# Kernel tuning notes

Measured on AMD Instinct MI355X. Metric: run time of the kernel, lower is better.

## Reference

```python
import jax, jax.numpy as jnp
import numpy as np

B, S, D, O = 1, 2048, 512, 512
H, QD, K, PK = 8, 256, 16, 256
N = PK * PK  # 65536 experts
HALF = QD // 2  # sub-query dim per product-key dimension


def _l2norm(x):
    # matches F.normalize(dim=-1): x / max(||x||, 1e-12)
    n = jnp.sqrt(jnp.sum(x * x, axis=-1, keepdims=True))
    return x / jnp.maximum(n, 1e-12)


def setup_inputs() -> dict:
    key = jax.random.key(0)
    ks = jax.random.split(key, 9)
    return {
        "hidden_states": jax.random.normal(ks[0], (B, S, D), jnp.float32),
        "Wq": jax.random.normal(ks[1], (H * QD, D), jnp.float32) * 0.02,
        "bq": jnp.zeros((H * QD,), jnp.float32),
        "ln_g": jnp.ones((QD,), jnp.float32),
        "ln_b": jnp.zeros((QD,), jnp.float32),
        "keys0": jax.random.normal(ks[2], (PK, HALF), jnp.float32) * 0.02,
        "keys1": jax.random.normal(ks[3], (PK, HALF), jnp.float32) * 0.02,
        "expert_down": jax.random.normal(ks[4], (N, D), jnp.float32) * 0.02,
        "expert_up": jax.random.normal(ks[5], (N, O), jnp.float32) * 0.02,
    }


def reference(hidden_states, Wq, bq, ln_g, ln_b, keys0, keys1, expert_down, expert_up):
    b, s, d = hidden_states.shape
    # query projection + layernorm over query_dim
    q = (hidden_states @ Wq.T + bq).reshape(b, s, H, QD)
    mu = jnp.mean(q, axis=-1, keepdims=True)
    var = jnp.mean((q - mu) ** 2, axis=-1, keepdims=True)
    q = (q - mu) / jnp.sqrt(var + 1e-5) * ln_g + ln_b
    # split into per-dimension sub-queries, normalize queries and keys
    q0, q1 = q[..., :HALF], q[..., HALF:]
    s0 = jnp.einsum('bshq,eq->bshe', _l2norm(q0), _l2norm(keys0))  # [b,s,H,PK]
    s1 = jnp.einsum('bshq,eq->bshe', _l2norm(q1), _l2norm(keys1))
    # per-dim top-k' (k' = K=16 here due to clamping logic in source)
    sc0, ix0 = jax.lax.top_k(s0, K)
    sc1, ix1 = jax.lax.top_k(s1, K)
    # combinatorial merge: scores add; NOTE source adds indices with multiplier 1
    # for the last dim and never scales the first-dim indices (faithful repro).
    cs = (sc0[..., :, None] + sc1[..., None, :]).reshape(b, s, H, K * K)
    ci = (ix0[..., :, None] + ix1[..., None, :]).reshape(b, s, H, K * K)
    fs, pos = jax.lax.top_k(cs, K)
    fi = jnp.take_along_axis(ci, pos, axis=-1)  # [b,s,H,K] expert ids
    w = jax.nn.softmax(fs, axis=-1)
    # gather rank-1 experts and apply: down-project, gelu, up-project, combine
    down = expert_down[fi]  # [b,s,H,K,D]
    up = expert_up[fi]      # [b,s,H,K,O]
    inner = jnp.einsum('bsd,bshkd->bshk', hidden_states, down)
    act = jax.nn.gelu(inner, approximate=False)
    out = jnp.einsum('bshk,bshko->bso', act * w, up)
    return out
```

## Files before the change

kernel.cpp:

```cpp
#include <hip/hip_runtime.h>
#include <math.h>

constexpr int Sx    = 2048;
constexpr int Dx    = 512;
constexpr int Hx    = 8;
constexpr int QDx   = 256;
constexpr int HALFx = 128;
constexpr int PKx   = 256;
constexpr int Kx    = 16;
constexpr int HQx   = Hx * QDx;
constexpr int Rx    = Sx * Hx;
constexpr int Ox    = 512;
constexpr int NEXP  = 511;

__device__ __forceinline__ unsigned short f2bf(float x) {
    unsigned u = __float_as_uint(x);
    unsigned r = (u + 0x7FFFu + ((u >> 16) & 1u)) >> 16;
    return (unsigned short)r;
}
__device__ __forceinline__ float bf2f(unsigned short h) {
    return __uint_as_float(((unsigned)h) << 16);
}

__global__ __launch_bounds__(64) void knorm_kernel(
    const float* __restrict__ k0, const float* __restrict__ k1,
    float* __restrict__ k0n, float* __restrict__ k1n)
{
    const int row = blockIdx.x;
    const float* src = (row < PKx) ? (k0 + (size_t)row * HALFx)
                                   : (k1 + (size_t)(row - PKx) * HALFx);
    float* dst = (row < PKx) ? (k0n + (size_t)row * HALFx)
                             : (k1n + (size_t)(row - PKx) * HALFx);
    const int t = threadIdx.x;
    float a = src[t];
    float b = src[t + 64];
    float ss = a * a + b * b;
#pragma unroll
    for (int off = 32; off; off >>= 1) ss += __shfl_xor(ss, off);
    float n = fmaxf(sqrtf(ss), 1e-12f);
    dst[t]      = a / n;
    dst[t + 64] = b / n;
}

__global__ __launch_bounds__(256) void conv_kernel(
    const float* __restrict__ src, unsigned short* __restrict__ dst, int n4)
{
    int i = blockIdx.x * 256 + threadIdx.x;
    if (i >= n4) return;
    float4 v = ((const float4*)src)[i];
    ((ushort4*)dst)[i] = make_ushort4(f2bf(v.x), f2bf(v.y), f2bf(v.z), f2bf(v.w));
}

__global__ __launch_bounds__(256) void gemm128_kernel(
    const float* __restrict__ A, int lda,
    const float* __restrict__ B, int ldb,
    const float* __restrict__ bias,
    float* __restrict__ C, int ldc, int K)
{
    constexpr int BM = 128, BN = 64, BK = 32;
    constexpr int ASTR = BM + 4;
    constexpr int BSTR = BN + 4;
    __shared__ __align__(16) float As[BK * ASTR];
    __shared__ __align__(16) float Bs[BK * BSTR];
    const int tid = threadIdx.x;
    const int bm = blockIdx.y * BM;
    const int bn = blockIdx.x * BN;

    const int sq = tid & 7;
    const int sr = tid >> 3;
    const int m0 = (tid >> 4) * 8;
    const int n0 = (tid & 15) * 4;

    float4 pa[4], pb[2];
#pragma unroll
    for (int i = 0; i < 4; ++i)
        pa[i] = *(const float4*)&A[(size_t)(bm + sr + i * 32) * lda + sq * 4];
#pragma unroll
    for (int i = 0; i < 2; ++i)
        pb[i] = *(const float4*)&B[(size_t)(bn + sr + i * 32) * ldb + sq * 4];

    float acc[8][4] = {{0.f}};
    const int niter = K / BK;
    for (int it = 0; it < niter; ++it) {
        __syncthreads();
#pragma unroll
        for (int i = 0; i < 4; ++i) {
            const float v[4] = {pa[i].x, pa[i].y, pa[i].z, pa[i].w};
#pragma unroll
            for (int j = 0; j < 4; ++j)
                As[(sq * 4 + j) * ASTR + sr + i * 32] = v[j];
        }
#pragma unroll
        for (int i = 0; i < 2; ++i) {
            const float v[4] = {pb[i].x, pb[i].y, pb[i].z, pb[i].w};
#pragma unroll
            for (int j = 0; j < 4; ++j)
                Bs[(sq * 4 + j) * BSTR + sr + i * 32] = v[j];
        }
        __syncthreads();
        if (it + 1 < niter) {
            const int ko = (it + 1) * BK;
#pragma unroll
            for (int i = 0; i < 4; ++i)
                pa[i] = *(const float4*)&A[(size_t)(bm + sr + i * 32) * lda + ko + sq * 4];
#pragma unroll
            for (int i = 0; i < 2; ++i)
                pb[i] = *(const float4*)&B[(size_t)(bn + sr + i * 32) * ldb + ko + sq * 4];
        }
#pragma unroll
        for (int k = 0; k < BK; ++k) {
            float af[8], bf[4];
            *(float4*)&af[0] = *(const float4*)&As[k * ASTR + m0];
            *(float4*)&af[4] = *(const float4*)&As[k * ASTR + m0 + 4];
            *(float4*)&bf[0] = *(const float4*)&Bs[k * BSTR + n0];
#pragma unroll
            for (int i = 0; i < 8; ++i)
#pragma unroll
                for (int j = 0; j < 4; ++j)
                    acc[i][j] = fmaf(af[i], bf[j], acc[i][j]);
        }
    }
    float4 bv = make_float4(0.f, 0.f, 0.f, 0.f);
    if (bias) bv = *(const float4*)&bias[bn + n0];
#pragma unroll
    for (int i = 0; i < 8; ++i) {
        float4 o;
        o.x = acc[i][0] + bv.x;
        o.y = acc[i][1] + bv.y;
        o.z = acc[i][2] + bv.z;
        o.w = acc[i][3] + bv.w;
        *(float4*)&C[(size_t)(bm + m0 + i) * ldc + bn + n0] = o;
    }
}

__global__ __launch_bounds__(256) void ln_kernel(
    float* __restrict__ q, const float* __restrict__ g,
    const float* __restrict__ b)
{
    const int r = blockIdx.x * 4 + (threadIdx.x >> 6);
    float* row = q + (size_t)r * QDx;
    const int t = threadIdx.x & 63;
    float v0 = row[t], v1 = row[t + 64], v2 = row[t + 128], v3 = row[t + 192];
    float sum = v0 + v1 + v2 + v3;
#pragma unroll
    for (int off = 32; off; off >>= 1) sum += __shfl_xor(sum, off);
    const float mu = sum * (1.f / 256.f);
    float d0 = v0 - mu, d1 = v1 - mu, d2 = v2 - mu, d3 = v3 - mu;
    float ss = d0 * d0 + d1 * d1 + d2 * d2 + d3 * d3;
#pragma unroll
    for (int off = 32; off; off >>= 1) ss += __shfl_xor(ss, off);
    const float var = ss * (1.f / 256.f);
    const float inv = 1.0f / sqrtf(var + 1e-5f);
    v0 = d0 * inv * g[t]       + b[t];
    v1 = d1 * inv * g[t + 64]  + b[t + 64];
    v2 = d2 * inv * g[t + 128] + b[t + 128];
    v3 = d3 * inv * g[t + 192] + b[t + 192];
    float s0 = v0 * v0 + v1 * v1;
#pragma unroll
    for (int off = 32; off; off >>= 1) s0 += __shfl_xor(s0, off);
    float n0 = fmaxf(sqrtf(s0), 1e-12f);
    float s1 = v2 * v2 + v3 * v3;
#pragma unroll
    for (int off = 32; off; off >>= 1) s1 += __shfl_xor(s1, off);
    float n1 = fmaxf(sqrtf(s1), 1e-12f);
    row[t]       = v0 / n0;
    row[t + 64]  = v1 / n0;
    row[t + 128] = v2 / n1;
    row[t + 192] = v3 / n1;
}

__device__ __forceinline__ unsigned fkey(float f) {
    unsigned u = __float_as_uint(f);
    return u ^ ((u & 0x80000000u) ? 0xFFFFFFFFu : 0x80000000u);
}

__device__ __forceinline__ void extract16(
    const float v[4], const unsigned u[4], unsigned T, int lane,
    unsigned long long lmask, float* outv, int* outi)
{
    unsigned long long mg[4];
    int gt_total = 0;
#pragma unroll
    for (int j = 0; j < 4; ++j) {
        mg[j] = __ballot(u[j] > T);
        gt_total += __popcll(mg[j]);
    }
    int bg = 0, be = gt_total;
#pragma unroll
    for (int j = 0; j < 4; ++j) {
        unsigned long long me = __ballot(u[j] == T);
        int idx = lane + 64 * j;
        if (u[j] > T) {
            int pg = bg + __popcll(mg[j] & lmask);
            outv[pg] = v[j]; outi[pg] = idx;
        } else if (u[j] == T) {
            int pe = be + __popcll(me & lmask);
            if (pe < 16) { outv[pe] = v[j]; outi[pe] = idx; }
        }
        bg += __popcll(mg[j]);
        be += __popcll(me);
    }
}

__global__ __launch_bounds__(256) void topk_kernel(
    const float* __restrict__ s0g, const float* __restrict__ s1g,
    int* __restrict__ fib, float* __restrict__ wb)
{
    __shared__ float sc0[4][Kx], sc1[4][Kx], fsv[4][Kx];
    __shared__ int ix0[4][Kx], ix1[4][Kx], fid[4][Kx];
    const int w = threadIdx.x >> 6;
    const int r = blockIdx.x * 4 + w;
    const int lane = threadIdx.x & 63;
    const unsigned long long lmask = (1ull << lane) - 1ull;

    float v0[4], v1[4];
    unsigned u0[4], u1[4];
#pragma unroll
    for (int j = 0; j < 4; ++j) {
        v0[j] = s0g[(size_t)r * PKx + lane + 64 * j];
        v1[j] = s1g[(size_t)r * PKx + lane + 64 * j];
        u0[j] = fkey(v0[j]);
        u1[j] = fkey(v1[j]);
    }

    unsigned T0 = 0, T1 = 0;
    for (int bit = 31; bit >= 0; --bit) {
        const unsigned c0 = T0 | (1u << bit);
        const unsigned c1 = T1 | (1u << bit);
        int n0 = 0, n1 = 0;
#pragma unroll
        for (int j = 0; j < 4; ++j) {
            n0 += __popcll(__ballot(u0[j] >= c0));
            n1 += __popcll(__ballot(u1[j] >= c1));
        }
        if (n0 >= Kx) T0 = c0;
        if (n1 >= Kx) T1 = c1;
    }
    extract16(v0, u0, T0, lane, lmask, &sc0[w][0], &ix0[w][0]);
    extract16(v1, u1, T1, lane, lmask, &sc1[w][0], &ix1[w][0]);
    __syncthreads();

    float cv[4];
    unsigned cu[4];
    int ci[4];
#pragma unroll
    for (int j = 0; j < 4; ++j) {
        int p = lane + 64 * j;
        cv[j] = sc0[w][p >> 4] + sc1[w][p & 15];
        cu[j] = fkey(cv[j]);
        ci[j] = ix0[w][p >> 4] + ix1[w][p & 15];
    }
    unsigned T2 = 0;
    for (int bit = 31; bit >= 0; --bit) {
        const unsigned c2 = T2 | (1u << bit);
        int n2 = 0;
#pragma unroll
        for (int j = 0; j < 4; ++j) n2 += __popcll(__ballot(cu[j] >= c2));
        if (n2 >= Kx) T2 = c2;
    }
    {
        unsigned long long mg[4];
        int gt_total = 0;
#pragma unroll
        for (int j = 0; j < 4; ++j) {
            mg[j] = __ballot(cu[j] > T2);
            gt_total += __popcll(mg[j]);
        }
        int bg = 0, be = gt_total;
#pragma unroll
        for (int j = 0; j < 4; ++j) {
            unsigned long long me = __ballot(cu[j] == T2);
            if (cu[j] > T2) {
                int pg = bg + __popcll(mg[j] & lmask);
                fsv[w][pg] = cv[j]; fid[w][pg] = ci[j];
            } else if (cu[j] == T2) {
                int pe = be + __popcll(me & lmask);
                if (pe < 16) { fsv[w][pe] = cv[j]; fid[w][pe] = ci[j]; }
            }
            bg += __popcll(mg[j]);
            be += __popcll(me);
        }
    }
    __syncthreads();

    float f = fsv[w][lane & 15];
    float mx = f;
#pragma unroll
    for (int off = 8; off; off >>= 1) mx = fmaxf(mx, __shfl_xor(mx, off, 16));
    float e = expf(f - mx);
    float sum = e;
#pragma unroll
    for (int off = 8; off; off >>= 1) sum += __shfl_xor(sum, off, 16);
    if (lane < Kx) {
        fib[(size_t)r * Kx + lane] = fid[w][lane];
        wb[(size_t)r * Kx + lane]  = e / sum;
    }
}

__global__ __launch_bounds__(256) void expert_kernel(
    const float* __restrict__ hidden,
    const unsigned short* __restrict__ downb,
    const unsigned short* __restrict__ upb,
    const int* __restrict__ fib,
    const float* __restrict__ wb, float* __restrict__ out)
{
    __shared__ float aw[Hx * Kx];
    __shared__ int fis[Hx * Kx];
    __shared__ float part[4][Ox];
    const int s = blockIdx.x;
    const int tid = threadIdx.x;
    const int wv = tid >> 6;
    const int lane = tid & 63;
    if (tid < Hx * Kx) fis[tid] = fib[(size_t)s * (Hx * Kx) + tid];
    float h8[8];
    {
        float4 a = *(const float4*)&hidden[(size_t)s * Dx + lane * 8];
        float4 b = *(const float4*)&hidden[(size_t)s * Dx + lane * 8 + 4];
        h8[0] = a.x; h8[1] = a.y; h8[2] = a.z; h8[3] = a.w;
        h8[4] = b.x; h8[5] = b.y; h8[6] = b.z; h8[7] = b.w;
    }
    __syncthreads();
    for (int p = wv; p < Hx * Kx; p += 4) {
        const unsigned short* dr = downb + (size_t)fis[p] * Dx + lane * 8;
        int4 d = *(const int4*)dr;
        float acc = 0.f;
        acc = fmaf(h8[0], bf2f((unsigned short)(d.x)),       acc);
        acc = fmaf(h8[1], bf2f((unsigned short)(d.x >> 16)), acc);
        acc = fmaf(h8[2], bf2f((unsigned short)(d.y)),       acc);
        acc = fmaf(h8[3], bf2f((unsigned short)(d.y >> 16)), acc);
        acc = fmaf(h8[4], bf2f((unsigned short)(d.z)),       acc);
        acc = fmaf(h8[5], bf2f((unsigned short)(d.z >> 16)), acc);
        acc = fmaf(h8[6], bf2f((unsigned short)(d.w)),       acc);
        acc = fmaf(h8[7], bf2f((unsigned short)(d.w >> 16)), acc);
#pragma unroll
        for (int off = 32; off; off >>= 1) acc += __shfl_xor(acc, off);
        if (lane == 0) {
            float x = acc;
            float act = 0.5f * x * (1.f + erff(x * 0.70710678118654752f));
            aw[p] = act * wb[(size_t)s * (Hx * Kx) + p];
        }
    }
    __syncthreads();
    float a8[8] = {0.f, 0.f, 0.f, 0.f, 0.f, 0.f, 0.f, 0.f};
    const int o0 = lane * 8;
    for (int p = wv * 32; p < wv * 32 + 32; ++p) {
        const float a = aw[p];
        const unsigned short* ur = upb + (size_t)fis[p] * Ox + o0;
        int4 u = *(const int4*)ur;
        a8[0] = fmaf(a, bf2f((unsigned short)(u.x)),       a8[0]);
        a8[1] = fmaf(a, bf2f((unsigned short)(u.x >> 16)), a8[1]);
        a8[2] = fmaf(a, bf2f((unsigned short)(u.y)),       a8[2]);
        a8[3] = fmaf(a, bf2f((unsigned short)(u.y >> 16)), a8[3]);
        a8[4] = fmaf(a, bf2f((unsigned short)(u.z)),       a8[4]);
        a8[5] = fmaf(a, bf2f((unsigned short)(u.z >> 16)), a8[5]);
        a8[6] = fmaf(a, bf2f((unsigned short)(u.w)),       a8[6]);
        a8[7] = fmaf(a, bf2f((unsigned short)(u.w >> 16)), a8[7]);
    }
    *(float4*)&part[wv][o0]     = make_float4(a8[0], a8[1], a8[2], a8[3]);
    *(float4*)&part[wv][o0 + 4] = make_float4(a8[4], a8[5], a8[6], a8[7]);
    __syncthreads();
    float r0 = part[0][tid] + part[1][tid] + part[2][tid] + part[3][tid];
    float r1 = part[0][tid + 256] + part[1][tid + 256]
             + part[2][tid + 256] + part[3][tid + 256];
    out[(size_t)s * Ox + tid]       = r0;
    out[(size_t)s * Ox + tid + 256] = r1;
}

extern "C" void kernel_launch(void* const* d_in, const int* in_sizes, int n_in,
                              void* d_out, int out_size, void* d_ws, size_t ws_size,
                              hipStream_t stream)
{
    const float* hidden = (const float*)d_in[0];
    const float* Wq     = (const float*)d_in[1];
    const float* bq     = (const float*)d_in[2];
    const float* ln_g   = (const float*)d_in[3];
    const float* ln_b   = (const float*)d_in[4];
    const float* keys0  = (const float*)d_in[5];
    const float* keys1  = (const float*)d_in[6];
    const float* edown  = (const float*)d_in[7];
    const float* eup    = (const float*)d_in[8];
    float* out = (float*)d_out;

    char* w = (char*)d_ws;
    float* q    = (float*)w;   w += (size_t)Sx * HQx * 4;
    float* k0n  = (float*)w;   w += (size_t)PKx * HALFx * 4;
    float* k1n  = (float*)w;   w += (size_t)PKx * HALFx * 4;
    float* s0   = (float*)w;   w += (size_t)Rx * PKx * 4;
    float* s1   = (float*)w;   w += (size_t)Rx * PKx * 4;
    float* wb   = (float*)w;   w += (size_t)Rx * Kx * 4;
    int*   fib  = (int*)w;     w += (size_t)Rx * Kx * 4;
    unsigned short* downb = (unsigned short*)w; w += (size_t)NEXP * Dx * 2 + 64;
    unsigned short* upb   = (unsigned short*)w; w += (size_t)NEXP * Ox * 2 + 64;

    const int nconv4 = NEXP * Dx / 4;

    hipLaunchKernelGGL(knorm_kernel, dim3(2 * PKx), dim3(64), 0, stream,
                       keys0, keys1, k0n, k1n);
    hipLaunchKernelGGL(conv_kernel, dim3((nconv4 + 255) / 256), dim3(256), 0, stream,
                       edown, downb, nconv4);
    hipLaunchKernelGGL(conv_kernel, dim3((nconv4 + 255) / 256), dim3(256), 0, stream,
                       eup, upb, nconv4);
    hipLaunchKernelGGL(gemm128_kernel, dim3(HQx / 64, Sx / 128), dim3(256), 0, stream,
                       hidden, Dx, Wq, Dx, bq, q, HQx, Dx);
    hipLaunchKernelGGL(ln_kernel, dim3(Rx / 4), dim3(256), 0, stream, q, ln_g, ln_b);
    hipLaunchKernelGGL(gemm128_kernel, dim3(PKx / 64, Rx / 128), dim3(256), 0, stream,
                       q, QDx, k0n, HALFx, (const float*)nullptr, s0, PKx, HALFx);
    hipLaunchKernelGGL(gemm128_kernel, dim3(PKx / 64, Rx / 128), dim3(256), 0, stream,
                       q + HALFx, QDx, k1n, HALFx, (const float*)nullptr, s1, PKx, HALFx);
    hipLaunchKernelGGL(topk_kernel, dim3(Rx / 4), dim3(256), 0, stream, s0, s1, fib, wb);
    hipLaunchKernelGGL(expert_kernel, dim3(Sx), dim3(256), 0, stream,
                       hidden, downb, upb, fib, wb, out);
}
```

Baseline: 414.4 us.

## Split-K the query GEMM, batch score GEMMs via grid z, merge conversion kernels

The query projection GEMM is split along K into two halves using a z grid dimension, and the halves are summed with the bias inside the layernorm kernel, which now writes to a separate buffer. The two score GEMMs are merged into one launch through the z dimension, and the two bf16 conversion kernels become a single launch. The expert down-projection is restructured so each 8-lane group handles one expert row over 64 contiguous elements, with hidden states staged in shared memory, which cuts shuffle reductions. The cost is extra workspace for the partial sums and one more full pass of memory traffic through the layernorm.

```diff
diff --git a/kernel.cpp b/kernel.cpp
--- a/kernel.cpp
+++ b/kernel.cpp
@@ -43,25 +43,35 @@
 }
 
 __global__ __launch_bounds__(256) void conv_kernel(
-    const float* __restrict__ src, unsigned short* __restrict__ dst, int n4)
+    const float* __restrict__ down, unsigned short* __restrict__ downb,
+    const float* __restrict__ up, unsigned short* __restrict__ upb, int n4)
 {
     int i = blockIdx.x * 256 + threadIdx.x;
-    if (i >= n4) return;
-    float4 v = ((const float4*)src)[i];
-    ((ushort4*)dst)[i] = make_ushort4(f2bf(v.x), f2bf(v.y), f2bf(v.z), f2bf(v.w));
-}
-
-__global__ __launch_bounds__(256) void gemm128_kernel(
-    const float* __restrict__ A, int lda,
-    const float* __restrict__ B, int ldb,
-    const float* __restrict__ bias,
-    float* __restrict__ C, int ldc, int K)
+    if (i >= 2 * n4) return;
+    const float* src = (i < n4) ? down : up;
+    unsigned short* dst = (i < n4) ? downb : upb;
+    int j = (i < n4) ? i : i - n4;
+    float4 v = ((const float4*)src)[j];
+    ((ushort4*)dst)[j] = make_ushort4(f2bf(v.x), f2bf(v.y), f2bf(v.z), f2bf(v.w));
+}
+
+__global__ __launch_bounds__(256) void gemm_z_kernel(
+    const float* __restrict__ A, int lda, int aoff_mult,
+    const float* __restrict__ B0, const float* __restrict__ B1, int ldb,
+    float* __restrict__ C0, float* __restrict__ C1, int ldc,
+    int K, int koff_mult)
 {
     constexpr int BM = 128, BN = 64, BK = 32;
     constexpr int ASTR = BM + 4;
     constexpr int BSTR = BN + 4;
     __shared__ __align__(16) float As[BK * ASTR];
     __shared__ __align__(16) float Bs[BK * BSTR];
+    const int z = blockIdx.z;
+    const float* B = z ? B1 : B0;
+    float* C = z ? C1 : C0;
+    A += (size_t)z * (aoff_mult + koff_mult);
+    B += (size_t)z * koff_mult;
+
     const int tid = threadIdx.x;
     const int bm = blockIdx.y * BM;
     const int bn = blockIdx.x * BN;
@@ -120,27 +130,28 @@
                     acc[i][j] = fmaf(af[i], bf[j], acc[i][j]);
         }
     }
-    float4 bv = make_float4(0.f, 0.f, 0.f, 0.f);
-    if (bias) bv = *(const float4*)&bias[bn + n0];
 #pragma unroll
     for (int i = 0; i < 8; ++i) {
-        float4 o;
-        o.x = acc[i][0] + bv.x;
-        o.y = acc[i][1] + bv.y;
-        o.z = acc[i][2] + bv.z;
-        o.w = acc[i][3] + bv.w;
+        float4 o = make_float4(acc[i][0], acc[i][1], acc[i][2], acc[i][3]);
         *(float4*)&C[(size_t)(bm + m0 + i) * ldc + bn + n0] = o;
     }
 }
 
 __global__ __launch_bounds__(256) void ln_kernel(
-    float* __restrict__ q, const float* __restrict__ g,
-    const float* __restrict__ b)
+    const float* __restrict__ q0, const float* __restrict__ q1,
+    const float* __restrict__ bq,
+    const float* __restrict__ g, const float* __restrict__ b,
+    float* __restrict__ qn)
 {
     const int r = blockIdx.x * 4 + (threadIdx.x >> 6);
-    float* row = q + (size_t)r * QDx;
+    const float* row0 = q0 + (size_t)r * QDx;
+    const float* row1 = q1 + (size_t)r * QDx;
     const int t = threadIdx.x & 63;
-    float v0 = row[t], v1 = row[t + 64], v2 = row[t + 128], v3 = row[t + 192];
+    const int cb = (r & 7) * QDx;
+    float v0 = row0[t]       + row1[t]       + bq[cb + t];
+    float v1 = row0[t + 64]  + row1[t + 64]  + bq[cb + t + 64];
+    float v2 = row0[t + 128] + row1[t + 128] + bq[cb + t + 128];
+    float v3 = row0[t + 192] + row1[t + 192] + bq[cb + t + 192];
     float sum = v0 + v1 + v2 + v3;
 #pragma unroll
     for (int off = 32; off; off >>= 1) sum += __shfl_xor(sum, off);
@@ -163,6 +174,7 @@
 #pragma unroll
     for (int off = 32; off; off >>= 1) s1 += __shfl_xor(s1, off);
     float n1 = fmaxf(sqrtf(s1), 1e-12f);
+    float* row = qn + (size_t)r * QDx;
     row[t]       = v0 / n0;
     row[t + 64]  = v1 / n0;
     row[t + 128] = v2 / n1;
@@ -304,6 +316,7 @@
     const int* __restrict__ fib,
     const float* __restrict__ wb, float* __restrict__ out)
 {
+    __shared__ float hsp[8 * 68];
     __shared__ float aw[Hx * Kx];
     __shared__ int fis[Hx * Kx];
     __shared__ float part[4][Ox];
@@ -312,35 +325,43 @@
     const int wv = tid >> 6;
     const int lane = tid & 63;
     if (tid < Hx * Kx) fis[tid] = fib[(size_t)s * (Hx * Kx) + tid];
-    float h8[8];
-    {
-        float4 a = *(const float4*)&hidden[(size_t)s * Dx + lane * 8];
-        float4 b = *(const float4*)&hidden[(size_t)s * Dx + lane * 8 + 4];
-        h8[0] = a.x; h8[1] = a.y; h8[2] = a.z; h8[3] = a.w;
-        h8[4] = b.x; h8[5] = b.y; h8[6] = b.z; h8[7] = b.w;
-    }
+#pragma unroll
+    for (int c = tid; c < Dx; c += 256)
+        hsp[(c >> 6) * 68 + (c & 63)] = hidden[(size_t)s * Dx + c];
     __syncthreads();
-    for (int p = wv; p < Hx * Kx; p += 4) {
-        const unsigned short* dr = downb + (size_t)fis[p] * Dx + lane * 8;
-        int4 d = *(const int4*)dr;
+
+    const int sub = lane & 7;
+    const int pl  = lane >> 3;
+    const float* hc = &hsp[sub * 68];
+    for (int pb = wv * 32; pb < wv * 32 + 32; pb += 8) {
+        const int p = pb + pl;
+        const unsigned short* dr = downb + (size_t)fis[p] * Dx + sub * 64;
         float acc = 0.f;
-        acc = fmaf(h8[0], bf2f((unsigned short)(d.x)),       acc);
-        acc = fmaf(h8[1], bf2f((unsigned short)(d.x >> 16)), acc);
-        acc = fmaf(h8[2], bf2f((unsigned short)(d.y)),       acc);
-        acc = fmaf(h8[3], bf2f((unsigned short)(d.y >> 16)), acc);
-        acc = fmaf(h8[4], bf2f((unsigned short)(d.z)),       acc);
-        acc = fmaf(h8[5], bf2f((unsigned short)(d.z >> 16)), acc);
-        acc = fmaf(h8[6], bf2f((unsigned short)(d.w)),       acc);
-        acc = fmaf(h8[7], bf2f((unsigned short)(d.w >> 16)), acc);
-#pragma unroll
-        for (int off = 32; off; off >>= 1) acc += __shfl_xor(acc, off);
-        if (lane == 0) {
+#pragma unroll
+        for (int j = 0; j < 8; ++j) {
+            int4 d = *(const int4*)(dr + j * 8);
+            float4 ha = *(const float4*)&hc[j * 8];
+            float4 hb = *(const float4*)&hc[j * 8 + 4];
+            acc = fmaf(ha.x, bf2f((unsigned short)(d.x)),       acc);
+            acc = fmaf(ha.y, bf2f((unsigned short)(d.x >> 16)), acc);
+            acc = fmaf(ha.z, bf2f((unsigned short)(d.y)),       acc);
+            acc = fmaf(ha.w, bf2f((unsigned short)(d.y >> 16)), acc);
+            acc = fmaf(hb.x, bf2f((unsigned short)(d.z)),       acc);
+            acc = fmaf(hb.y, bf2f((unsigned short)(d.z >> 16)), acc);
+            acc = fmaf(hb.z, bf2f((unsigned short)(d.w)),       acc);
+            acc = fmaf(hb.w, bf2f((unsigned short)(d.w >> 16)), acc);
+        }
+        acc += __shfl_xor(acc, 1);
+        acc += __shfl_xor(acc, 2);
+        acc += __shfl_xor(acc, 4);
+        if (sub == 0) {
             float x = acc;
             float act = 0.5f * x * (1.f + erff(x * 0.70710678118654752f));
             aw[p] = act * wb[(size_t)s * (Hx * Kx) + p];
         }
     }
     __syncthreads();
+
     float a8[8] = {0.f, 0.f, 0.f, 0.f, 0.f, 0.f, 0.f, 0.f};
     const int o0 = lane * 8;
     for (int p = wv * 32; p < wv * 32 + 32; ++p) {
@@ -382,7 +403,9 @@
     float* out = (float*)d_out;
 
     char* w = (char*)d_ws;
-    float* q    = (float*)w;   w += (size_t)Sx * HQx * 4;
+    float* q0   = (float*)w;   w += (size_t)Sx * HQx * 4;
+    float* q1   = (float*)w;   w += (size_t)Sx * HQx * 4;
+    float* qn   = (float*)w;   w += (size_t)Sx * HQx * 4;
     float* k0n  = (float*)w;   w += (size_t)PKx * HALFx * 4;
     float* k1n  = (float*)w;   w += (size_t)PKx * HALFx * 4;
     float* s0   = (float*)w;   w += (size_t)Rx * PKx * 4;
@@ -396,17 +419,14 @@
 
     hipLaunchKernelGGL(knorm_kernel, dim3(2 * PKx), dim3(64), 0, stream,
                        keys0, keys1, k0n, k1n);
-    hipLaunchKernelGGL(conv_kernel, dim3((nconv4 + 255) / 256), dim3(256), 0, stream,
-                       edown, downb, nconv4);
-    hipLaunchKernelGGL(conv_kernel, dim3((nconv4 + 255) / 256), dim3(256), 0, stream,
-                       eup, upb, nconv4);
-    hipLaunchKernelGGL(gemm128_kernel, dim3(HQx / 64, Sx / 128), dim3(256), 0, stream,
-                       hidden, Dx, Wq, Dx, bq, q, HQx, Dx);
-    hipLaunchKernelGGL(ln_kernel, dim3(Rx / 4), dim3(256), 0, stream, q, ln_g, ln_b);
-    hipLaunchKernelGGL(gemm128_kernel, dim3(PKx / 64, Rx / 128), dim3(256), 0, stream,
-                       q, QDx, k0n, HALFx, (const float*)nullptr, s0, PKx, HALFx);
-    hipLaunchKernelGGL(gemm128_kernel, dim3(PKx / 64, Rx / 128), dim3(256), 0, stream,
-                       q + HALFx, QDx, k1n, HALFx, (const float*)nullptr, s1, PKx, HALFx);
+    hipLaunchKernelGGL(conv_kernel, dim3((2 * nconv4 + 255) / 256), dim3(256), 0, stream,
+                       edown, downb, eup, upb, nconv4);
+    hipLaunchKernelGGL(gemm_z_kernel, dim3(HQx / 64, Sx / 128, 2), dim3(256), 0, stream,
+                       hidden, Dx, 0, Wq, Wq, Dx, q0, q1, HQx, Dx / 2, Dx / 2);
+    hipLaunchKernelGGL(ln_kernel, dim3(Rx / 4), dim3(256), 0, stream,
+                       q0, q1, bq, ln_g, ln_b, qn);
+    hipLaunchKernelGGL(gemm_z_kernel, dim3(PKx / 64, Rx / 128, 2), dim3(256), 0, stream,
+                       qn, QDx, HALFx, k0n, k1n, HALFx, s0, s1, PKx, HALFx, 0);
     hipLaunchKernelGGL(topk_kernel, dim3(Rx / 4), dim3(256), 0, stream, s0, s1, fib, wb);
     hipLaunchKernelGGL(expert_kernel, dim3(Sx), dim3(256), 0, stream,
                        hidden, downb, upb, fib, wb, out);
```

Result: no change. 409.3 us (-1.2%).
